# Optimization experiments

Hardware: AMD Instinct MI355X
Metric: run time of the kernel (lower is better)

Reference implementation:

```python
import jax, jax.numpy as jnp
import numpy as np

V, L, H, D = 2048, 16, 8, 64   # vocab, max_chars, n_head, word_vec_d
B = 8192                        # number of words in batch (rows of char_code)
NW_TOTAL = 8192                 # len(word_code)
N_NAMES = 2048                  # total names (4 words each)
N_GROUPS = 8                    # groups of names (256 each)
PAD = 0
TEMP = D ** 0.5
LN_EPS = 1e-5


def make_pos():
    freq = D // 2
    inv = 1.0 / np.power(10000.0, np.arange(freq) / freq)
    ph = np.outer(np.arange(L), inv)
    return jnp.asarray(np.hstack([np.cos(ph), np.sin(ph)]).astype(np.float32))


def setup_inputs() -> dict:
    key = jax.random.key(0)
    ks = jax.random.split(key, 8)
    char_emb = jax.random.normal(ks[0], (V, D), jnp.float32) * 0.02
    char_emb = char_emb.at[PAD].set(0.0)  # padding_idx row
    Wc = jax.random.normal(ks[1], (D, 3 * H * D), jnp.float32) * 0.02
    bc = jnp.zeros((3 * H * D,), jnp.float32)
    Wp = jax.random.normal(ks[2], (D, 3 * H * D), jnp.float32) * 0.02
    bp = jnp.zeros((3 * H * D,), jnp.float32)
    gamma = jnp.ones((D,), jnp.float32)
    beta = jnp.zeros((D,), jnp.float32)
    W1 = jax.random.normal(ks[3], (H, 16), jnp.float32) * 0.1
    b1 = jnp.zeros((16,), jnp.float32)
    W2 = jax.random.normal(ks[4], (16, 8), jnp.float32) * 0.1
    b2 = jnp.zeros((8,), jnp.float32)
    char_code = jax.random.randint(ks[5], (B, L), 1, V)
    char_code = char_code.at[::4, -2:].set(PAD)  # some padded tails
    word_code = jax.random.randint(ks[6], (NW_TOTAL,), 0, B)
    n_words = np.full((N_NAMES,), NW_TOTAL // N_NAMES, dtype=np.int64)
    n_names = np.full((N_GROUPS,), N_NAMES // N_GROUPS, dtype=np.int64)
    return {"char_emb": char_emb, "Wc": Wc, "bc": bc, "Wp": Wp, "bp": bp,
            "gamma": gamma, "beta": beta, "W1": W1, "b1": b1, "W2": W2, "b2": b2,
            "char_code": char_code, "word_code": word_code,
            "n_words": n_words, "n_names": n_names}


def reference(char_emb, Wc, bc, Wp, bp, gamma, beta, W1, b1, W2, b2,
              char_code, word_code, n_words, n_names):
    pos = make_pos()
    # ComputeQKV: linear d -> 3*H*d, reshape [N,3,H,D]
    cqkv = (char_emb @ Wc + bc).reshape(V, 3, H, D)
    cq, ck, cv = cqkv[:, 0], cqkv[:, 1], cqkv[:, 2]        # [V,H,D]
    pqkv = (pos @ Wp + bp).reshape(L, 3, H, D)
    pq, pk, pv = pqkv[:, 0], pqkv[:, 1], pqkv[:, 2]        # [L,H,D]
    # precomputed score tables
    char_qk = jnp.einsum('xhd,yhd->hxy', cq, ck).at[:, :, PAD].set(-1e9)  # [H,V,V]
    pos_qk = jnp.einsum('xhd,yhd->hxy', pq, pk)                            # [H,L,L]
    # char_q@pos_k + (pos_q@char_k)^T summed over the first dim of char_pos_qk
    cp = jnp.einsum('vhd,lhd->hvl', cq, pk) + jnp.einsum('lhd,vhd->hvl', pq, ck)  # [H,V,L]
    code = char_code                                        # [B,L]
    # gather-assembled scores, no [H,B*L,V] intermediate
    sim = (char_qk[:, code[:, :, None], code[:, None, :]]   # [H,B,L,L]
           + cp[:, code]
           + pos_qk[:, None]) / TEMP
    attn = jax.nn.softmax(sim, axis=-1)                     # [H,B,L,L] (dropout=0)
    v = jnp.transpose(cv[code], (2, 0, 1, 3)) + pv.transpose(1, 0, 2)[:, None]  # [H,B,L,D]
    out = jnp.einsum('hbij,hbjd->bihd', attn, v)            # [B,L,H,D]
    mu = out.mean(-1, keepdims=True)
    var = out.var(-1, keepdims=True)
    out = (out - mu) / jnp.sqrt(var + LN_EPS) * gamma + beta  # LayerNorm(D)
    char_ft = jnp.transpose(out, (0, 2, 1, 3))              # [B,H,L,D]
    mask = (code != PAD)
    pooled = jnp.einsum('bl,bhld->bhd', mask.astype(out.dtype), char_ft) \
             / mask.sum(-1)[:, None, None]                  # masked mean over chars
    x = jnp.transpose(pooled, (0, 2, 1))                    # [B,D,H]
    x = jax.nn.relu(x @ W1 + b1) @ W2 + b2                  # MLP over head dim -> [B,D,8]
    word_ft = x.reshape(B, -1)[word_code]                   # [NW_TOTAL, D*8]
    nw = np.asarray(n_words)
    seg = jnp.asarray(np.repeat(np.arange(nw.size), nw))
    name_ft = jax.ops.segment_sum(word_ft, seg, num_segments=nw.size) \
              / jnp.asarray(nw, word_ft.dtype)[:, None]     # ragged mean -> [N_NAMES, D*8]
    splits = np.cumsum(np.asarray(n_names))[:-1]
    return tuple(jnp.split(name_ft, splits, axis=0))
```

## Files before the change

### kernel.cpp

```cpp
#include <hip/hip_runtime.h>
#include <hip/hip_bf16.h>
#include <math.h>

typedef __attribute__((ext_vector_type(8))) short bfrag;
typedef __attribute__((ext_vector_type(4))) float ffrag;
typedef __attribute__((ext_vector_type(4))) float f4v;

#define C3 1536
#define PS 24

__device__ __forceinline__ unsigned short f2bf(float f) {
    unsigned u = __float_as_uint(f);
    return (unsigned short)((u + 0x7FFFu + ((u >> 16) & 1u)) >> 16);
}
__device__ __forceinline__ float bf2f(unsigned short s) {
    return __uint_as_float(((unsigned)s) << 16);
}

__device__ __forceinline__ float row16_sum(float x) {
    int v;
    v = __builtin_amdgcn_update_dpp(0, __float_as_int(x), 0xB1, 0xF, 0xF, true);
    x += __int_as_float(v);
    v = __builtin_amdgcn_update_dpp(0, __float_as_int(x), 0x4E, 0xF, 0xF, true);
    x += __int_as_float(v);
    v = __builtin_amdgcn_update_dpp(0, __float_as_int(x), 0x124, 0xF, 0xF, true);
    x += __int_as_float(v);
    v = __builtin_amdgcn_update_dpp(0, __float_as_int(x), 0x128, 0xF, 0xF, true);
    x += __int_as_float(v);
    return x;
}

__global__ __launch_bounds__(256) void precompute_kernel(
    const float* __restrict__ char_emb, const float* __restrict__ Wc, const float* __restrict__ bc,
    const float* __restrict__ Wp, const float* __restrict__ bp,
    const float* __restrict__ gamma, const float* __restrict__ beta,
    unsigned short* __restrict__ cqkv, float* __restrict__ pqkv,
    unsigned short* __restrict__ pbf, float* __restrict__ gbtab)
{
    const int b = blockIdx.x;
    const int t = threadIdx.x;
    if (b < 1536) {
        const int mt = b / 6;
        const int nt = b - mt * 6;
        const int m0 = mt * 8;
        const int c = nt * 256 + t;
        const float qs = (c < 512) ? 0.125f : 1.f;
        const float bias = bc[c];
        float acc[8];
        #pragma unroll
        for (int r = 0; r < 8; ++r) acc[r] = bias;
        #pragma unroll 16
        for (int dd = 0; dd < 64; ++dd) {
            const float wv = Wc[dd * C3 + c];
            #pragma unroll
            for (int r = 0; r < 8; ++r)
                acc[r] = fmaf(char_emb[(m0 + r) * 64 + dd], wv, acc[r]);
        }
        #pragma unroll
        for (int r = 0; r < 8; ++r)
            cqkv[(size_t)(m0 + r) * C3 + c] = f2bf(acc[r] * qs);
    } else {
        const int e = b - 1536;
        const int l = e / 6;
        const int cc = e - l * 6;
        if (b == 1536 && t < 64) {
            #pragma unroll
            for (int dt = 0; dt < 4; ++dt) {
                gbtab[t * 8 + dt]     = gamma[dt * 16 + t];
                gbtab[t * 8 + 4 + dt] = beta[dt * 16 + t];
            }
        }
        __shared__ float spos[64];
        if (t < 64) {
            const int f = t & 31;
            const float inv = exp2f(-(float)f * 0.41524101186092034f);
            const float ph = (float)l * inv;
            spos[t] = (t < 32) ? cosf(ph) : sinf(ph);
        }
        __syncthreads();
        const int c = t + cc * 256;
        float acc = bp[c];
        #pragma unroll
        for (int dd = 0; dd < 64; ++dd)
            acc = fmaf(spos[dd], Wp[dd * C3 + c], acc);
        pqkv[l * C3 + c] = acc;
        if (c < 1024) {
            const float qs = (c < 512) ? 0.125f : 1.f;
            pbf[(c >> 6) * 1024 + l * 64 + (c & 63)] = f2bf(acc * qs);
        }
    }
}

__global__ __launch_bounds__(256) void vprime_kernel(
    const unsigned short* __restrict__ cqkv, const float* __restrict__ pqkv,
    unsigned short* __restrict__ vtab, float* __restrict__ posqk)
{
    const int c = blockIdx.x;
    const int t = threadIdx.x;
    if (c >= 2048) {
        const int h = c - 2048;
        const int i = t >> 4, j = t & 15;
        const f4v* qa = (const f4v*)(pqkv + i * C3 + h * 64);
        const f4v* kb = (const f4v*)(pqkv + j * C3 + 512 + h * 64);
        float acc = 0.f;
        #pragma unroll
        for (int x = 0; x < 16; ++x) {
            const f4v a = qa[x], bb = kb[x];
            acc = fmaf(a[0], bb[0], acc);
            acc = fmaf(a[1], bb[1], acc);
            acc = fmaf(a[2], bb[2], acc);
            acc = fmaf(a[3], bb[3], acc);
        }
        posqk[h * 256 + (i >> 2) * 64 + j * 4 + (i & 3)] = acc * 0.125f;
        return;
    }
    const int hd8 = t & 63;
    const int l0 = t >> 6;
    const bfrag cv = *(const bfrag*)(cqkv + (size_t)c * C3 + 1024 + hd8 * 8);
    #pragma unroll
    for (int li = 0; li < 4; ++li) {
        const int l = l0 + li * 4;
        const f4v pa = *(const f4v*)(pqkv + l * C3 + 1024 + hd8 * 8);
        const f4v pb = *(const f4v*)(pqkv + l * C3 + 1024 + hd8 * 8 + 4);
        bfrag o;
        #pragma unroll
        for (int j = 0; j < 8; ++j)
            o[j] = (short)f2bf(bf2f((unsigned short)cv[j]) + ((j < 4) ? pa[j] : pb[j - 4]));
        *(bfrag*)(vtab + ((size_t)c * 16 + l) * 512 + hd8 * 8) = o;
    }
}

__global__ __launch_bounds__(256, 8) void attn_kernel(
    const unsigned short* __restrict__ cqkv, const unsigned short* __restrict__ pbf,
    const unsigned short* __restrict__ vtab, const int* __restrict__ char_code,
    const float* __restrict__ posqk, const float* __restrict__ gbtab,
    float* __restrict__ pooled)
{
    __shared__ __attribute__((aligned(16))) unsigned short sVt[4 * 1024];
    __shared__ __attribute__((aligned(16))) unsigned short sP[4 * 16 * PS];

    const int t = threadIdx.x;
    const int lane = t & 63;
    const int wid = t >> 6;
    const int gw = blockIdx.x * 4 + wid;
    const int w = gw >> 3;
    const int h = gw & 7;
    const int quad = lane >> 4;
    const int n = lane & 15;

    const int code = char_code[w * 16 + n];
    const bool kvalid = (code != 0);
    const unsigned long long msk = __ballot(kvalid);
    const int nv = __popcll(msk & 0xFFFFull);

    const f4v g4 = *(const f4v*)(gbtab + n * 8);
    const f4v b4 = *(const f4v*)(gbtab + n * 8 + 4);

    unsigned short* vt = sVt + wid * 1024;
    #pragma unroll
    for (int cc = 0; cc < 2; ++cc) {
        const int d8 = quad + cc * 4;
        const bfrag vb = *(const bfrag*)(vtab + ((size_t)code * 16 + n) * 512 + h * 64 + d8 * 8);
        #pragma unroll
        for (int j = 0; j < 8; ++j) {
            const int d = d8 * 8 + j;
            const int e = ((d >> 4) * 2 + (n >> 3)) * 128
                        + ((d & 15) ^ ((n >> 3) << 2)) * 8 + (n & 7);
            vt[e] = (unsigned short)vb[j];
        }
    }

    ffrag accS = *(const ffrag*)(posqk + h * 256 + quad * 64 + n * 4);
    {
        const unsigned short* cbase = cqkv + (size_t)code * C3 + h * 64;
        const unsigned short* pq = pbf + h * 1024 + n * 64;
        const unsigned short* pk = pbf + (8 + h) * 1024 + n * 64;
        #pragma unroll
        for (int cc = 0; cc < 2; ++cc) {
            const int off = quad * 8 + cc * 32;
            const bfrag cqF = *(const bfrag*)(cbase + off);
            const bfrag ckF = *(const bfrag*)(cbase + 512 + off);
            const bfrag pqF = *(const bfrag*)(pq + off);
            const bfrag pkF = *(const bfrag*)(pk + off);
            accS = __builtin_amdgcn_mfma_f32_16x16x32_bf16(cqF, ckF, accS, 0, 0, 0);
            accS = __builtin_amdgcn_mfma_f32_16x16x32_bf16(cqF, pkF, accS, 0, 0, 0);
            accS = __builtin_amdgcn_mfma_f32_16x16x32_bf16(ckF, pqF, accS, 0, 0, 0);
        }
    }

    unsigned short* pt = sP + wid * 16 * PS;
    #pragma unroll
    for (int r = 0; r < 4; ++r) {
        const float pr = kvalid ? __expf(accS[r]) : 0.f;
        pt[(quad * 4 + r) * PS + n] = f2bf(pr);
    }

    bfrag ap;
    #pragma unroll
    for (int j = 0; j < 8; ++j) ap[j] = 0;
    if (quad < 2) ap = *(const bfrag*)(pt + n * PS + quad * 8);
    const int q2 = quad & 1;
    ffrag accO[4];
    #pragma unroll
    for (int dt = 0; dt < 4; ++dt) { ffrag z = {0.f,0.f,0.f,0.f}; accO[dt] = z; }
    #pragma unroll
    for (int dt = 0; dt < 4; ++dt) {
        const bfrag bv = *(const bfrag*)(vt + (dt * 2 + q2) * 128 + (n ^ (q2 << 2)) * 8);
        accO[dt] = __builtin_amdgcn_mfma_f32_16x16x32_bf16(ap, bv, accO[dt], 0, 0, 0);
    }
    bfrag onesf;
    #pragma unroll
    for (int j = 0; j < 8; ++j) onesf[j] = (short)0x3F80;
    ffrag accE = {0.f, 0.f, 0.f, 0.f};
    accE = __builtin_amdgcn_mfma_f32_16x16x32_bf16(ap, onesf, accE, 0, 0, 0);

    float ps1[4], ps2[4];
    #pragma unroll
    for (int r = 0; r < 4; ++r) {
        ps1[r] = accO[0][r] + accO[1][r] + accO[2][r] + accO[3][r];
        ps2[r] = accO[0][r]*accO[0][r] + accO[1][r]*accO[1][r]
               + accO[2][r]*accO[2][r] + accO[3][r]*accO[3][r];
        ps1[r] = row16_sum(ps1[r]);
        ps2[r] = row16_sum(ps2[r]);
    }
    float pool[4] = {0.f, 0.f, 0.f, 0.f};
    #pragma unroll
    for (int r = 0; r < 4; ++r) {
        const float mu   = ps1[r] * 0.015625f;
        const float var  = fmaxf(ps2[r] * 0.015625f - mu * mu, 0.f);
        const float rstd = rsqrtf(var + accE[r] * accE[r] * 1e-5f);
        const float iv = ((msk >> (quad * 4 + r)) & 1ull) ? 1.f : 0.f;
        #pragma unroll
        for (int dt = 0; dt < 4; ++dt)
            pool[dt] += iv * fmaf((accO[dt][r] - mu) * rstd, g4[dt], b4[dt]);
    }
    #pragma unroll
    for (int xm = 16; xm <= 32; xm <<= 1) {
        #pragma unroll
        for (int dt = 0; dt < 4; ++dt) pool[dt] += __shfl_xor(pool[dt], xm);
    }
    if (quad == 0) {
        const float invnv = 1.f / (float)nv;
        f4v o;
        #pragma unroll
        for (int dt = 0; dt < 4; ++dt) o[dt] = pool[dt] * invnv;
        *(f4v*)(pooled + (size_t)w * 512 + h * 64 + n * 4) = o;
    }
}

__global__ __launch_bounds__(128) void mlp_avg_kernel(
    const float* __restrict__ pooled, const int* __restrict__ word_code,
    const int* __restrict__ n_words,
    const float* __restrict__ W1, const float* __restrict__ b1,
    const float* __restrict__ W2, const float* __restrict__ b2,
    float* __restrict__ out)
{
    __shared__ float sPool[512];
    __shared__ float sHid[64 * 17];
    __shared__ float sWb[280];
    __shared__ int sred[128];
    const int nm = blockIdx.x;
    const int t = threadIdx.x;
    sWb[t] = W1[t];
    sWb[144 + t] = W2[t];
    if (t < 16) sWb[128 + t] = b1[t];
    if (t < 8)  sWb[272 + t] = b2[t];

    int part = 0;
    for (int i = t; i < nm; i += 128) part += n_words[i];
    sred[t] = part;
    __syncthreads();
    for (int s = 64; s > 0; s >>= 1) {
        if (t < s) sred[t] += sred[t + s];
        __syncthreads();
    }
    const int off = sred[0];
    const int cnt = n_words[nm];

    const int d = t & 63, o4 = (t >> 6) * 4;
    const int dmap = (d & 15) * 4 + (d >> 4);
    float xacc[4] = {0.f, 0.f, 0.f, 0.f};

    for (int r = 0; r < cnt; ++r) {
        const int wc = word_code[off + r];
        __syncthreads();
        *(f4v*)(sPool + t * 4) = *(const f4v*)(pooled + (size_t)wc * 512 + t * 4);
        __syncthreads();
        if (t < 64) {
            float pl[8];
            #pragma unroll
            for (int hh = 0; hh < 8; ++hh) pl[hh] = sPool[hh * 64 + dmap];
            #pragma unroll
            for (int c = 0; c < 16; ++c) {
                float hs = sWb[128 + c];
                #pragma unroll
                for (int hh = 0; hh < 8; ++hh) hs = fmaf(pl[hh], sWb[hh * 16 + c], hs);
                sHid[t * 17 + c] = fmaxf(hs, 0.f);
            }
        }
        __syncthreads();
        #pragma unroll
        for (int c = 0; c < 16; ++c) {
            const float hc = sHid[d * 17 + c];
            #pragma unroll
            for (int oo = 0; oo < 4; ++oo)
                xacc[oo] = fmaf(hc, sWb[144 + c * 8 + o4 + oo], xacc[oo]);
        }
    }
    const float inv = 1.f / (float)cnt;
    f4v res;
    #pragma unroll
    for (int oo = 0; oo < 4; ++oo) res[oo] = xacc[oo] * inv + sWb[272 + o4 + oo];
    *(f4v*)(out + (size_t)nm * 512 + d * 8 + o4) = res;
}

extern "C" void kernel_launch(void* const* d_in, const int* in_sizes, int n_in,
                              void* d_out, int out_size, void* d_ws, size_t ws_size,
                              hipStream_t stream) {
    (void)in_sizes; (void)n_in; (void)out_size; (void)ws_size;
    const float* char_emb = (const float*)d_in[0];
    const float* Wc    = (const float*)d_in[1];
    const float* bc    = (const float*)d_in[2];
    const float* Wp    = (const float*)d_in[3];
    const float* bp    = (const float*)d_in[4];
    const float* gamma = (const float*)d_in[5];
    const float* beta  = (const float*)d_in[6];
    const float* W1    = (const float*)d_in[7];
    const float* b1    = (const float*)d_in[8];
    const float* W2    = (const float*)d_in[9];
    const float* b2    = (const float*)d_in[10];
    const int* char_code = (const int*)d_in[11];
    const int* word_code = (const int*)d_in[12];
    const int* n_words   = (const int*)d_in[13];

    char* ws = (char*)d_ws;
    unsigned short* cqkv = (unsigned short*)ws;
    float* pqkv = (float*)(ws + 6291456);
    unsigned short* pbf  = (unsigned short*)(ws + 6389760);
    unsigned short* vtab = (unsigned short*)(ws + 6422528);
    float* pooled = (float*)(ws + 39976960);
    float* posqk  = (float*)(ws + 56754176);
    float* gbtab  = (float*)(ws + 56762368);
    float* out = (float*)d_out;

    precompute_kernel<<<1632, 256, 0, stream>>>(char_emb, Wc, bc, Wp, bp, gamma, beta,
                                                cqkv, pqkv, pbf, gbtab);
    vprime_kernel<<<2056, 256, 0, stream>>>(cqkv, pqkv, vtab, posqk);
    attn_kernel<<<16384, 256, 0, stream>>>(cqkv, pbf, vtab, char_code, posqk, gbtab, pooled);
    mlp_avg_kernel<<<2048, 128, 0, stream>>>(pooled, word_code, n_words,
                                             W1, b1, W2, b2, out);
}
```

Baseline: 205.1 us.

## Eliminate vprime kernel by fusing V-plus-position add and pos QK into attention

Removes the vprime kernel that materialized a per-character, per-position V table (about 32 MB) and the fp32 position QK table. The attention kernel now loads the char V and a bf16 position V, adds and rounds them while scattering into shared memory, and computes the pos-q times pos-k term with an extra MFMA instead of loading precomputed fp32 values. This saves a kernel launch plus a large table write and reread, at the cost of extra ALU and MFMA work per wave and slightly lower precision on the position terms.

```diff
diff --git a/kernel.cpp b/kernel.cpp
--- a/kernel.cpp
+++ b/kernel.cpp
@@ -34,8 +34,8 @@
     const float* __restrict__ char_emb, const float* __restrict__ Wc, const float* __restrict__ bc,
     const float* __restrict__ Wp, const float* __restrict__ bp,
     const float* __restrict__ gamma, const float* __restrict__ beta,
-    unsigned short* __restrict__ cqkv, float* __restrict__ pqkv,
-    unsigned short* __restrict__ pbf, float* __restrict__ gbtab)
+    unsigned short* __restrict__ cqkv, unsigned short* __restrict__ pbf,
+    float* __restrict__ gbtab)
 {
     const int b = blockIdx.x;
     const int t = threadIdx.x;
@@ -83,57 +83,14 @@
         #pragma unroll
         for (int dd = 0; dd < 64; ++dd)
             acc = fmaf(spos[dd], Wp[dd * C3 + c], acc);
-        pqkv[l * C3 + c] = acc;
-        if (c < 1024) {
-            const float qs = (c < 512) ? 0.125f : 1.f;
-            pbf[(c >> 6) * 1024 + l * 64 + (c & 63)] = f2bf(acc * qs);
-        }
-    }
-}
-
-__global__ __launch_bounds__(256) void vprime_kernel(
-    const unsigned short* __restrict__ cqkv, const float* __restrict__ pqkv,
-    unsigned short* __restrict__ vtab, float* __restrict__ posqk)
-{
-    const int c = blockIdx.x;
-    const int t = threadIdx.x;
-    if (c >= 2048) {
-        const int h = c - 2048;
-        const int i = t >> 4, j = t & 15;
-        const f4v* qa = (const f4v*)(pqkv + i * C3 + h * 64);
-        const f4v* kb = (const f4v*)(pqkv + j * C3 + 512 + h * 64);
-        float acc = 0.f;
-        #pragma unroll
-        for (int x = 0; x < 16; ++x) {
-            const f4v a = qa[x], bb = kb[x];
-            acc = fmaf(a[0], bb[0], acc);
-            acc = fmaf(a[1], bb[1], acc);
-            acc = fmaf(a[2], bb[2], acc);
-            acc = fmaf(a[3], bb[3], acc);
-        }
-        posqk[h * 256 + (i >> 2) * 64 + j * 4 + (i & 3)] = acc * 0.125f;
-        return;
-    }
-    const int hd8 = t & 63;
-    const int l0 = t >> 6;
-    const bfrag cv = *(const bfrag*)(cqkv + (size_t)c * C3 + 1024 + hd8 * 8);
-    #pragma unroll
-    for (int li = 0; li < 4; ++li) {
-        const int l = l0 + li * 4;
-        const f4v pa = *(const f4v*)(pqkv + l * C3 + 1024 + hd8 * 8);
-        const f4v pb = *(const f4v*)(pqkv + l * C3 + 1024 + hd8 * 8 + 4);
-        bfrag o;
-        #pragma unroll
-        for (int j = 0; j < 8; ++j)
-            o[j] = (short)f2bf(bf2f((unsigned short)cv[j]) + ((j < 4) ? pa[j] : pb[j - 4]));
-        *(bfrag*)(vtab + ((size_t)c * 16 + l) * 512 + hd8 * 8) = o;
+        const float qs = (c < 512) ? 0.125f : 1.f;
+        pbf[((c >> 9) * 8 + ((c >> 6) & 7)) * 1024 + l * 64 + (c & 63)] = f2bf(acc * qs);
     }
 }
 
 __global__ __launch_bounds__(256, 8) void attn_kernel(
     const unsigned short* __restrict__ cqkv, const unsigned short* __restrict__ pbf,
-    const unsigned short* __restrict__ vtab, const int* __restrict__ char_code,
-    const float* __restrict__ posqk, const float* __restrict__ gbtab,
+    const int* __restrict__ char_code, const float* __restrict__ gbtab,
     float* __restrict__ pooled)
 {
     __shared__ __attribute__((aligned(16))) unsigned short sVt[4 * 1024];
@@ -157,20 +114,27 @@
     const f4v b4 = *(const f4v*)(gbtab + n * 8 + 4);
 
     unsigned short* vt = sVt + wid * 1024;
-    #pragma unroll
-    for (int cc = 0; cc < 2; ++cc) {
-        const int d8 = quad + cc * 4;
-        const bfrag vb = *(const bfrag*)(vtab + ((size_t)code * 16 + n) * 512 + h * 64 + d8 * 8);
-        #pragma unroll
-        for (int j = 0; j < 8; ++j) {
-            const int d = d8 * 8 + j;
-            const int e = ((d >> 4) * 2 + (n >> 3)) * 128
-                        + ((d & 15) ^ ((n >> 3) << 2)) * 8 + (n & 7);
-            vt[e] = (unsigned short)vb[j];
-        }
-    }
-
-    ffrag accS = *(const ffrag*)(posqk + h * 256 + quad * 64 + n * 4);
+    {
+        const unsigned short* cvp = cqkv + (size_t)code * C3 + 1024 + h * 64;
+        const unsigned short* pvp = pbf + (16 + h) * 1024 + n * 64;
+        #pragma unroll
+        for (int cc = 0; cc < 2; ++cc) {
+            const int d8 = quad + cc * 4;
+            const bfrag cv = *(const bfrag*)(cvp + d8 * 8);
+            const bfrag pv = *(const bfrag*)(pvp + d8 * 8);
+            #pragma unroll
+            for (int j = 0; j < 8; ++j) {
+                const float f = bf2f((unsigned short)cv[j]) + bf2f((unsigned short)pv[j]);
+                const unsigned u = __float_as_uint(f) + 0x8000u;
+                const int d = d8 * 8 + j;
+                const int e = ((d >> 4) * 2 + (n >> 3)) * 128
+                            + ((d & 15) ^ ((n >> 3) << 2)) * 8 + (n & 7);
+                vt[e] = (unsigned short)(u >> 16);
+            }
+        }
+    }
+
+    ffrag accS = {0.f, 0.f, 0.f, 0.f};
     {
         const unsigned short* cbase = cqkv + (size_t)code * C3 + h * 64;
         const unsigned short* pq = pbf + h * 1024 + n * 64;
@@ -185,6 +149,7 @@
             accS = __builtin_amdgcn_mfma_f32_16x16x32_bf16(cqF, ckF, accS, 0, 0, 0);
             accS = __builtin_amdgcn_mfma_f32_16x16x32_bf16(cqF, pkF, accS, 0, 0, 0);
             accS = __builtin_amdgcn_mfma_f32_16x16x32_bf16(ckF, pqF, accS, 0, 0, 0);
+            accS = __builtin_amdgcn_mfma_f32_16x16x32_bf16(pqF, pkF, accS, 0, 0, 0);
         }
     }
 
@@ -335,18 +300,14 @@
 
     char* ws = (char*)d_ws;
     unsigned short* cqkv = (unsigned short*)ws;
-    float* pqkv = (float*)(ws + 6291456);
-    unsigned short* pbf  = (unsigned short*)(ws + 6389760);
-    unsigned short* vtab = (unsigned short*)(ws + 6422528);
-    float* pooled = (float*)(ws + 39976960);
-    float* posqk  = (float*)(ws + 56754176);
-    float* gbtab  = (float*)(ws + 56762368);
+    unsigned short* pbf  = (unsigned short*)(ws + 6291456);
+    float* pooled = (float*)(ws + 6340608);
+    float* gbtab  = (float*)(ws + 23117824);
     float* out = (float*)d_out;
 
     precompute_kernel<<<1632, 256, 0, stream>>>(char_emb, Wc, bc, Wp, bp, gamma, beta,
-                                                cqkv, pqkv, pbf, gbtab);
-    vprime_kernel<<<2056, 256, 0, stream>>>(cqkv, pqkv, vtab, posqk);
-    attn_kernel<<<16384, 256, 0, stream>>>(cqkv, pbf, vtab, char_code, posqk, gbtab, pooled);
+                                                cqkv, pbf, gbtab);
+    attn_kernel<<<16384, 256, 0, stream>>>(cqkv, pbf, char_code, gbtab, pooled);
     mlp_avg_kernel<<<2048, 128, 0, stream>>>(pooled, word_code, n_words,
                                              W1, b1, W2, b2, out);
 }
```

Result: slower. 214.1 us (+4.4%).
